# Kernel optimization log

Hardware: AMD Instinct MI355X
Metric: run time of the kernel (lower is better)

## Reference

```python
import jax, jax.numpy as jnp
import numpy as np

N = 100000      # total nodes across batched graphs
E = 1600000     # total edges (avg degree 16)
B = 4096        # number of graphs in the batch
DIM_IN = 74
D2 = 200
D3 = 12
H1 = 100        # gc1 output
DG = 20         # gc2 output (d_g)
M1 = 128
M2 = 32
FD = (DG + 1) * (D2 + 1)  # 4221 fusion features
EPS = 1e-5


def _glorot(k, shape):
    lim = float(np.sqrt(6.0 / (shape[0] + shape[1])))
    return jax.random.uniform(k, shape, jnp.float32, -lim, lim)


def setup_inputs() -> dict:
    key = jax.random.key(0)
    ks = jax.random.split(key, 18)
    inp = {
        'feat': jax.random.normal(ks[0], (N, DIM_IN), jnp.float32),
        'desc_2d': jax.random.normal(ks[1], (B, D2), jnp.float32),
        'desc_3d': jax.random.normal(ks[2], (B, D3), jnp.float32),
        'edge_src': jax.random.randint(ks[3], (E,), 0, N, jnp.int32),
        'edge_dst': jax.random.randint(ks[4], (E,), 0, N, jnp.int32),
        'graph_ids': jnp.sort(jax.random.randint(ks[5], (N,), 0, B, jnp.int32)),
        # GCN layer params (Linear inside NodeApplyModule)
        'W_gc1': _glorot(ks[6], (DIM_IN, H1)),
        'b_gc1': jnp.zeros((H1,), jnp.float32),
        'W_gc2': _glorot(ks[7], (H1, DG)),
        'b_gc2': jnp.zeros((DG,), jnp.float32),
        # attention weight W: (d_g, dim_2d_desc)
        'W_attn': _glorot(ks[8], (DG, D2)),
        # MLP
        'W_fc1': _glorot(ks[9], (FD, M1)),
        'b_fc1': jnp.zeros((M1,), jnp.float32),
        'W_fc2': _glorot(ks[10], (M1, M2)),
        'b_fc2': jnp.zeros((M2,), jnp.float32),
        'W_fc3': _glorot(ks[11], (M2, 1)),
        'b_fc3': jnp.zeros((1,), jnp.float32),
        # BatchNorm affine params
        'gamma1': jnp.ones((M1,), jnp.float32),
        'beta1': jnp.zeros((M1,), jnp.float32),
        'gamma2': jnp.ones((M2,), jnp.float32),
        'beta2': jnp.zeros((M2,), jnp.float32),
    }
    return inp


def _mean_agg(h, src, dst):
    # copy_u('h','m') then mean over mailbox; zero in-degree nodes keep h (DGL semantics)
    msg = h[src]                                                   # [E, d] gather
    s = jax.ops.segment_sum(msg, dst, num_segments=N)              # [N, d]
    deg = jax.ops.segment_sum(jnp.ones((src.shape[0],), h.dtype), dst, num_segments=N)
    mean = s / jnp.maximum(deg, 1.0)[:, None]
    return jnp.where((deg > 0)[:, None], mean, h)


def _batchnorm(x, gamma, beta):
    mu = jnp.mean(x, axis=0)
    var = jnp.mean(jnp.square(x - mu), axis=0)  # biased var (training mode)
    return (x - mu) * jax.lax.rsqrt(var + EPS) * gamma + beta


def reference(feat, desc_2d, desc_3d, edge_src, edge_dst, graph_ids,
              W_gc1, b_gc1, W_gc2, b_gc2, W_attn,
              W_fc1, b_fc1, W_fc2, b_fc2, W_fc3, b_fc3,
              gamma1, beta1, gamma2, beta2):
    # GCN layer 1: mean neighbor agg -> linear -> relu
    h = jax.nn.relu(_mean_agg(feat, edge_src, edge_dst) @ W_gc1 + b_gc1)   # [N, 100]
    # GCN layer 2
    h = jax.nn.relu(_mean_agg(h, edge_src, edge_dst) @ W_gc2 + b_gc2)      # [N, 20]
    # dgl.mean_nodes: per-graph mean readout
    sg = jax.ops.segment_sum(h, graph_ids, num_segments=B)                 # [B, 20]
    cnt = jax.ops.segment_sum(jnp.ones((N,), h.dtype), graph_ids, num_segments=B)
    hg = sg / jnp.maximum(cnt, 1.0)[:, None]                               # [B, 20]
    # attention over 2D descriptors
    attn = jax.nn.softmax(hg @ W_attn, axis=-1)                            # [B, 200]
    desc_att = attn * desc_2d
    # augment with ones and take outer product (bmm fusion)
    ones = jnp.ones((hg.shape[0], 1), hg.dtype)
    hg_a = jnp.concatenate([hg, ones], axis=1)                             # [B, 21]
    da_a = jnp.concatenate([desc_att, ones], axis=1)                       # [B, 201]
    fusion = jnp.einsum('bi,bj->bij', hg_a, da_a).reshape(hg.shape[0], -1) # [B, 4221]
    # MLP with BatchNorm (training-mode stats, dropout off)
    out = jax.nn.relu(_batchnorm(fusion @ W_fc1 + b_fc1, gamma1, beta1))
    out = jax.nn.relu(_batchnorm(out @ W_fc2 + b_fc2, gamma2, beta2))
    out = out @ W_fc3 + b_fc3                                              # [B, 1]
    return out
```

## Files before the change

### kernel.cpp

```cpp
#include <hip/hip_runtime.h>

#define NN 100000
#define NE 1600000
#define NB 4096
#define DIN 74
#define DPAD 80
#define DH1 100
#define DGD 20
#define DD2 200
#define DM1 128
#define DM2 32
#define NSEG 8
#define KPAD 4352
#define KSEG 544
#define NBUK 64
#define BNODES 1563
#define CAP 26500
#define EPB 3125
typedef unsigned int uint;
typedef unsigned short ushort;
typedef __attribute__((ext_vector_type(8))) short bf16x8;
typedef __attribute__((ext_vector_type(4))) float f32x4;

__device__ __forceinline__ float bf2f(ushort u){ return __uint_as_float(((uint)u)<<16); }
__device__ __forceinline__ ushort f2bf(float f){
  uint u = __float_as_uint(f);
  return (ushort)((u + 0x7fffu + ((u >> 16) & 1u)) >> 16);
}
__device__ __forceinline__ uint bucket_of(int d){
  return (uint)(((unsigned long long)(uint)d * 2747900ull) >> 32);
}
__device__ __forceinline__ void acc2u(float2& a, uint v){
  a.x += __uint_as_float(v << 16);
  a.y += __uint_as_float(v & 0xffff0000u);
}
__device__ __forceinline__ void acc8(float4& a, float4& b, uint4 v){
  a.x += __uint_as_float(v.x << 16);
  a.y += __uint_as_float(v.x & 0xffff0000u);
  a.z += __uint_as_float(v.y << 16);
  a.w += __uint_as_float(v.y & 0xffff0000u);
  b.x += __uint_as_float(v.z << 16);
  b.y += __uint_as_float(v.z & 0xffff0000u);
  b.z += __uint_as_float(v.w << 16);
  b.w += __uint_as_float(v.w & 0xffff0000u);
}

__global__ void k_cvt(const float* __restrict__ feat, const int* __restrict__ gid,
                      ushort* __restrict__ fb, int* __restrict__ cntg){
  int idx = blockIdx.x*256 + threadIdx.x;
  if(idx < NN*DPAD){
    int row = idx / DPAD, d = idx - row*DPAD;
    fb[idx] = (d < DIN) ? f2bf(feat[(size_t)row*DIN + d]) : (ushort)0;
  }
  if(idx < NN) atomicAdd(&cntg[gid[idx]], 1);
}

__global__ __launch_bounds__(256) void k_bucket2(const int* __restrict__ src,
      const int* __restrict__ dst, int* __restrict__ bukCur, uint2* __restrict__ pairs){
  __shared__ uint2 stage[EPB];
  __shared__ ushort bidx[EPB];
  __shared__ int cnt[NBUK], lofs[NBUK], gadj[NBUK], cur[NBUK];
  int tid = threadIdx.x;
  if(tid < NBUK) cnt[tid] = 0;
  __syncthreads();
  int e0 = blockIdx.x * EPB;
  for(int i = tid; i < EPB; i += 256)
    atomicAdd(&cnt[bucket_of(dst[e0 + i])], 1);
  __syncthreads();
  if(tid == 0){
    int acc = 0;
    #pragma unroll
    for(int b=0;b<NBUK;b++){ lofs[b] = acc; acc += cnt[b]; }
  }
  __syncthreads();
  if(tid < NBUK){
    int base = atomicAdd(&bukCur[tid], cnt[tid]);
    gadj[tid] = tid*CAP + base - lofs[tid];
    cur[tid]  = lofs[tid];
  }
  __syncthreads();
  for(int i = tid; i < EPB; i += 256){
    int d = dst[e0 + i];
    int s = src[e0 + i];
    uint b = bucket_of(d);
    int p = atomicAdd(&cur[b], 1);
    stage[p] = make_uint2((uint)s, (uint)d);
    bidx[p] = (ushort)b;
  }
  __syncthreads();
  for(int i = tid; i < EPB; i += 256)
    pairs[(size_t)gadj[bidx[i]] + i] = stage[i];
}

__global__ __launch_bounds__(512) void k_csr(const uint2* __restrict__ pairs,
      const int* __restrict__ bukTot, int* __restrict__ rowptr, int* __restrict__ adj){
  __shared__ int degL[BNODES];
  __shared__ int curL[BNODES];
  __shared__ int tsum[512];
  int b = blockIdx.x, tid = threadIdx.x;
  int d0 = b*BNODES;
  int nloc = min(BNODES, NN - d0);
  int gbase = 0;
  for(int i=0;i<b;i++) gbase += bukTot[i];
  int tot = bukTot[b];
  for(int i=tid;i<nloc;i+=512){ degL[i]=0; curL[i]=0; }
  __syncthreads();
  const uint2* pb = pairs + (size_t)b*CAP;
  for(int i=tid;i<tot;i+=512)
    atomicAdd(&degL[(int)pb[i].y - d0], 1);
  __syncthreads();
  int o0 = tid*4;
  int v0=0,v1=0,v2=0,v3=0,s=0;
  if(o0 < nloc){
    v0 = degL[o0];
    v1 = (o0+1<nloc)?degL[o0+1]:0;
    v2 = (o0+2<nloc)?degL[o0+2]:0;
    v3 = (o0+3<nloc)?degL[o0+3]:0;
    s = v0+v1+v2+v3;
  }
  tsum[tid]=s; __syncthreads();
  for(int off=1;off<512;off<<=1){
    int t2 = (tid>=off)?tsum[tid-off]:0;
    __syncthreads();
    tsum[tid]+=t2;
    __syncthreads();
  }
  int excl = tsum[tid]-s;
  if(o0 < nloc){
    int p0 = excl, p1 = p0+v0, p2 = p1+v1, p3 = p2+v2;
    degL[o0]=p0;
    rowptr[d0+o0]=gbase+p0;
    if(o0+1<nloc){ degL[o0+1]=p1; rowptr[d0+o0+1]=gbase+p1; }
    if(o0+2<nloc){ degL[o0+2]=p2; rowptr[d0+o0+2]=gbase+p2; }
    if(o0+3<nloc){ degL[o0+3]=p3; rowptr[d0+o0+3]=gbase+p3; }
  }
  if(b==NBUK-1 && tid==0) rowptr[NN]=gbase+tot;
  __syncthreads();
  for(int i=tid;i<tot;i+=512){
    uint2 pr = pb[i];
    int dl = (int)pr.y - d0;
    int pos = atomicAdd(&curL[dl],1);
    adj[gbase + degL[dl] + pos] = (int)pr.x;
  }
}

__global__ __launch_bounds__(512) void k_scan_g(const int* __restrict__ cntg,
                                                int* __restrict__ gofs){
  __shared__ int tsum[512];
  int tid = threadIdx.x;
  int o0 = tid*8;
  int v[8]; int s=0;
  #pragma unroll
  for(int j=0;j<8;j++){ v[j]=cntg[o0+j]; s+=v[j]; }
  tsum[tid]=s; __syncthreads();
  for(int off=1;off<512;off<<=1){
    int t=(tid>=off)?tsum[tid-off]:0;
    __syncthreads();
    tsum[tid]+=t;
    __syncthreads();
  }
  int acc = tsum[tid]-s;
  #pragma unroll
  for(int j=0;j<8;j++){ gofs[o0+j]=acc; acc+=v[j]; }
  if(tid==511) gofs[NB]=acc;
}

__global__ void k_agg1e(const ushort* __restrict__ fb, const float* __restrict__ feat,
                        const int* __restrict__ rowptr, const int* __restrict__ adj,
                        ushort* __restrict__ outb){
  int wid  = (blockIdx.x*blockDim.x + threadIdx.x) >> 6;
  int lane = threadIdx.x & 63;
  if(wid >= NN) return;
  int r0 = rowptr[wid], r1 = rowptr[wid+1];
  int eo = lane / 10;
  int part = lane - eo*10;
  bool act = lane < 60;
  if(!act){ eo = 0; part = 0; }
  float4 la0={0,0,0,0}, ha0={0,0,0,0}, la1={0,0,0,0}, ha1={0,0,0,0};
  float4 la2={0,0,0,0}, ha2={0,0,0,0}, la3={0,0,0,0}, ha3={0,0,0,0};
  for(int j = r0; j < r1; j += 24){
    int j0 = j + eo, j1 = j + 6 + eo, j2 = j + 12 + eo, j3 = j + 18 + eo;
    bool p0 = act && (j0 < r1), p1 = act && (j1 < r1);
    bool p2 = act && (j2 < r1), p3 = act && (j3 < r1);
    int s0 = adj[p0 ? j0 : r0];
    int s1 = adj[p1 ? j1 : r0];
    int s2 = adj[p2 ? j2 : r0];
    int s3 = adj[p3 ? j3 : r0];
    uint4 v0 = *(const uint4*)&fb[(size_t)s0*DPAD + part*8];
    uint4 v1 = *(const uint4*)&fb[(size_t)s1*DPAD + part*8];
    uint4 v2 = *(const uint4*)&fb[(size_t)s2*DPAD + part*8];
    uint4 v3 = *(const uint4*)&fb[(size_t)s3*DPAD + part*8];
    if(p0) acc8(la0, ha0, v0);
    if(p1) acc8(la1, ha1, v1);
    if(p2) acc8(la2, ha2, v2);
    if(p3) acc8(la3, ha3, v3);
  }
  float4 lo, hi;
  lo.x = (la0.x+la1.x)+(la2.x+la3.x); lo.y = (la0.y+la1.y)+(la2.y+la3.y);
  lo.z = (la0.z+la1.z)+(la2.z+la3.z); lo.w = (la0.w+la1.w)+(la2.w+la3.w);
  hi.x = (ha0.x+ha1.x)+(ha2.x+ha3.x); hi.y = (ha0.y+ha1.y)+(ha2.y+ha3.y);
  hi.z = (ha0.z+ha1.z)+(ha2.z+ha3.z); hi.w = (ha0.w+ha1.w)+(ha2.w+ha3.w);
  float4 L1,H1,L2,H2,L3,H3,L4,H4,L5,H5;
  #define SH4(dst,src,off) dst.x=__shfl(src.x,lane+off,64); dst.y=__shfl(src.y,lane+off,64); \
                           dst.z=__shfl(src.z,lane+off,64); dst.w=__shfl(src.w,lane+off,64);
  SH4(L1,lo,10) SH4(H1,hi,10)
  SH4(L2,lo,20) SH4(H2,hi,20)
  SH4(L3,lo,30) SH4(H3,hi,30)
  SH4(L4,lo,40) SH4(H4,hi,40)
  SH4(L5,lo,50) SH4(H5,hi,50)
  #undef SH4
  if(lane < 10){
    float4 tl, th;
    tl.x = ((lo.x+L1.x)+(L2.x+L3.x))+(L4.x+L5.x);
    tl.y = ((lo.y+L1.y)+(L2.y+L3.y))+(L4.y+L5.y);
    tl.z = ((lo.z+L1.z)+(L2.z+L3.z))+(L4.z+L5.z);
    tl.w = ((lo.w+L1.w)+(L2.w+L3.w))+(L4.w+L5.w);
    th.x = ((hi.x+H1.x)+(H2.x+H3.x))+(H4.x+H5.x);
    th.y = ((hi.y+H1.y)+(H2.y+H3.y))+(H4.y+H5.y);
    th.z = ((hi.z+H1.z)+(H2.z+H3.z))+(H4.z+H5.z);
    th.w = ((hi.w+H1.w)+(H2.w+H3.w))+(H4.w+H5.w);
    int d = r1 - r0;
    int dbase = part*8;
    if(d > 0){
      float inv = 1.f/(float)d;
      tl.x*=inv; tl.y*=inv; tl.z*=inv; tl.w*=inv;
      th.x*=inv; th.y*=inv; th.z*=inv; th.w*=inv;
    } else {
      const float* fr = feat + (size_t)wid*DIN;
      tl.x = (dbase+0 < DIN) ? fr[dbase+0] : 0.f;
      tl.y = (dbase+1 < DIN) ? fr[dbase+1] : 0.f;
      tl.z = (dbase+2 < DIN) ? fr[dbase+2] : 0.f;
      tl.w = (dbase+3 < DIN) ? fr[dbase+3] : 0.f;
      th.x = (dbase+4 < DIN) ? fr[dbase+4] : 0.f;
      th.y = (dbase+5 < DIN) ? fr[dbase+5] : 0.f;
      th.z = (dbase+6 < DIN) ? fr[dbase+6] : 0.f;
      th.w = (dbase+7 < DIN) ? fr[dbase+7] : 0.f;
    }
    uint4 o;
    o.x = (uint)f2bf(tl.x) | ((uint)f2bf(tl.y) << 16);
    o.y = (uint)f2bf(tl.z) | ((uint)f2bf(tl.w) << 16);
    o.z = (uint)f2bf(th.x) | ((uint)f2bf(th.y) << 16);
    o.w = (uint)f2bf(th.z) | ((uint)f2bf(th.w) << 16);
    *(uint4*)&outb[(size_t)wid*DPAD + dbase] = o;
  }
}

__global__ void k_prep_all(const float* __restrict__ Wf1, ushort* __restrict__ Bthi,
                           const float* __restrict__ W1g, ushort* __restrict__ W1tb,
                           const float* __restrict__ W2g, ushort* __restrict__ W2tb){
  int blk = blockIdx.x;
  int tid = threadIdx.x;
  if(blk < KPAD/32){
    __shared__ float Wl[32][128];
    int k0 = blk * 32;
    for(int idx=tid; idx<32*128; idx+=256){
      int kk = idx >> 7, n = idx & 127;
      int k = k0 + kk;
      Wl[kk][n] = (k < 4221) ? Wf1[(size_t)k*128 + n] : 0.f;
    }
    __syncthreads();
    int n = tid >> 1, kh = (tid & 1) * 16;
    uint ph[8];
    #pragma unroll
    for(int e=0;e<8;e++){
      ushort h0 = f2bf(Wl[kh+2*e][n]);
      ushort h1 = f2bf(Wl[kh+2*e+1][n]);
      ph[e] = (uint)h0 | ((uint)h1 << 16);
    }
    uint4* dh = (uint4*)(Bthi + (size_t)n*KPAD + k0 + kh);
    dh[0] = make_uint4(ph[0],ph[1],ph[2],ph[3]);
    dh[1] = make_uint4(ph[4],ph[5],ph[6],ph[7]);
  } else if(blk == KPAD/32){
    for(int idx = tid; idx < 112*96; idx += 256){
      int n = idx / 96, k = idx - n*96;
      float v = (n < DH1 && k < DIN) ? W1g[(size_t)k*DH1 + n] : 0.f;
      W1tb[idx] = f2bf(v);
    }
  } else {
    for(int idx = tid; idx < 32*128; idx += 256){
      int n = idx >> 7, k = idx & 127;
      float v = (n < DGD && k < DH1) ? W2g[(size_t)k*DGD + n] : 0.f;
      W2tb[idx] = f2bf(v);
    }
  }
}

__global__ __launch_bounds__(256) void k_gcn12(const ushort* __restrict__ Ab80,
      const ushort* __restrict__ W1tb, const ushort* __restrict__ W2tb,
      const float* __restrict__ b1, ushort* __restrict__ y2b){
  __shared__ ushort L[24960];
  ushort* As  = L;
  ushort* Ws  = L + 128*104;
  ushort* Hs  = L;
  ushort* W2s = L + 128*136;
  int tid = threadIdx.x;
  int n0 = blockIdx.x*128;
  #pragma unroll
  for(int p=0;p<5;p++){
    int idx = tid + p*256;
    int row = idx/10, c = (idx - row*10)*8;
    uint4 v = {0,0,0,0};
    if(n0+row < NN) v = *(const uint4*)&Ab80[(size_t)(n0+row)*DPAD + c];
    *(uint4*)&As[row*104 + c] = v;
  }
  { int row = tid>>1, c = 80 + (tid&1)*8;
    *(uint4*)&As[row*104 + c] = (uint4){0,0,0,0}; }
  #pragma unroll
  for(int p=0;p<6;p++){
    int idx = tid + p*256;
    if(idx < 1344){
      int row = idx/12, c = (idx - row*12)*8;
      *(uint4*)&Ws[row*104 + c] = *(const uint4*)&W1tb[row*96 + c];
    }
  }
  __syncthreads();
  int lane = tid & 63, w = tid >> 6;
  int wm = w*32;
  int frow = lane & 15, fk = (lane>>4)*8;
  f32x4 acc[2][7];
  #pragma unroll
  for(int a=0;a<2;a++)
    #pragma unroll
    for(int b=0;b<7;b++) acc[a][b] = (f32x4){0.f,0.f,0.f,0.f};
  #pragma unroll
  for(int ks=0; ks<3; ks++){
    bf16x8 af[2], bfr[7];
    #pragma unroll
    for(int mt=0;mt<2;mt++) af[mt] = *(const bf16x8*)&As[(wm+mt*16+frow)*104 + ks*32 + fk];
    #pragma unroll
    for(int nt=0;nt<7;nt++) bfr[nt] = *(const bf16x8*)&Ws[(nt*16+frow)*104 + ks*32 + fk];
    #pragma unroll
    for(int mt=0;mt<2;mt++)
      #pragma unroll
      for(int nt=0;nt<7;nt++)
        acc[mt][nt] = __builtin_amdgcn_mfma_f32_16x16x32_bf16(af[mt], bfr[nt], acc[mt][nt], 0, 0, 0);
  }
  int crow = (lane>>4)*4, ccol = lane & 15;
  float bv[7];
  #pragma unroll
  for(int nt=0;nt<7;nt++){
    int c = nt*16 + ccol;
    bv[nt] = (c < DH1) ? b1[c] : 0.f;
  }
  __syncthreads();
  #pragma unroll
  for(int mt=0;mt<2;mt++)
    #pragma unroll
    for(int nt=0;nt<7;nt++)
      #pragma unroll
      for(int rr=0;rr<4;rr++)
        Hs[(wm + mt*16 + crow + rr)*136 + nt*16 + ccol] =
            f2bf(fmaxf(acc[mt][nt][rr] + bv[nt], 0.f));
  { int row = tid>>1, c = 112 + (tid&1)*8;
    *(uint4*)&Hs[row*136 + c] = (uint4){0,0,0,0}; }
  #pragma unroll
  for(int p=0;p<2;p++){
    int idx = tid + p*256;
    int row = idx >> 4, c = (idx & 15)*8;
    *(uint4*)&W2s[row*136 + c] = *(const uint4*)&W2tb[row*128 + c];
  }
  __syncthreads();
  f32x4 acc2[2][2];
  #pragma unroll
  for(int a=0;a<2;a++){ acc2[a][0]=(f32x4){0,0,0,0}; acc2[a][1]=(f32x4){0,0,0,0}; }
  #pragma unroll
  for(int ks=0; ks<4; ks++){
    bf16x8 af2[2], bf2r[2];
    #pragma unroll
    for(int mt=0;mt<2;mt++) af2[mt] = *(const bf16x8*)&Hs[(wm+mt*16+frow)*136 + ks*32 + fk];
    #pragma unroll
    for(int nt=0;nt<2;nt++) bf2r[nt] = *(const bf16x8*)&W2s[(nt*16+frow)*136 + ks*32 + fk];
    #pragma unroll
    for(int mt=0;mt<2;mt++)
      #pragma unroll
      for(int nt=0;nt<2;nt++)
        acc2[mt][nt] = __builtin_amdgcn_mfma_f32_16x16x32_bf16(af2[mt], bf2r[nt], acc2[mt][nt], 0, 0, 0);
  }
  #pragma unroll
  for(int mt=0;mt<2;mt++)
    #pragma unroll
    for(int nt=0;nt<2;nt++)
      #pragma unroll
      for(int rr=0;rr<4;rr++){
        int col = nt*16 + ccol;
        int r = n0 + wm + mt*16 + crow + rr;
        if(col < DGD && r < NN)
          y2b[(size_t)r*DGD + col] = f2bf(acc2[mt][nt][rr]);
      }
}

__global__ void k_agg2d(const ushort* __restrict__ y2b, const int* __restrict__ rowptr,
                        const int* __restrict__ adj, const float* __restrict__ b2,
                        float* __restrict__ y3){
  int wid  = (blockIdx.x*blockDim.x + threadIdx.x) >> 6;
  int lane = threadIdx.x & 63;
  if(wid >= NN) return;
  int r0 = rowptr[wid], r1 = rowptr[wid+1];
  int eo = lane / 5;
  int part = lane - eo*5;
  bool act = lane < 60;
  if(!act){ eo = 0; part = 0; }
  float4 a0={0,0,0,0}, a1={0,0,0,0}, a2={0,0,0,0}, a3={0,0,0,0};
  for(int j = r0; j < r1; j += 48){
    int j0 = j + eo, j1 = j + 12 + eo, j2 = j + 24 + eo, j3 = j + 36 + eo;
    bool p0 = act && (j0 < r1), p1 = act && (j1 < r1);
    bool p2 = act && (j2 < r1), p3 = act && (j3 < r1);
    int s0 = adj[p0 ? j0 : r0];
    int s1 = adj[p1 ? j1 : r0];
    int s2 = adj[p2 ? j2 : r0];
    int s3 = adj[p3 ? j3 : r0];
    uint2 v0 = *(const uint2*)&y2b[(size_t)s0*DGD + part*4];
    uint2 v1 = *(const uint2*)&y2b[(size_t)s1*DGD + part*4];
    uint2 v2 = *(const uint2*)&y2b[(size_t)s2*DGD + part*4];
    uint2 v3 = *(const uint2*)&y2b[(size_t)s3*DGD + part*4];
    if(p0){ acc2u(*(float2*)&a0.x, v0.x); acc2u(*(float2*)&a0.z, v0.y); }
    if(p1){ acc2u(*(float2*)&a1.x, v1.x); acc2u(*(float2*)&a1.z, v1.y); }
    if(p2){ acc2u(*(float2*)&a2.x, v2.x); acc2u(*(float2*)&a2.z, v2.y); }
    if(p3){ acc2u(*(float2*)&a3.x, v3.x); acc2u(*(float2*)&a3.z, v3.y); }
  }
  float4 t;
  t.x = (a0.x+a1.x)+(a2.x+a3.x);
  t.y = (a0.y+a1.y)+(a2.y+a3.y);
  t.z = (a0.z+a1.z)+(a2.z+a3.z);
  t.w = (a0.w+a1.w)+(a2.w+a3.w);
  t.x += __shfl(t.x, lane+30, 64); t.y += __shfl(t.y, lane+30, 64);
  t.z += __shfl(t.z, lane+30, 64); t.w += __shfl(t.w, lane+30, 64);
  t.x += __shfl(t.x, lane+15, 64); t.y += __shfl(t.y, lane+15, 64);
  t.z += __shfl(t.z, lane+15, 64); t.w += __shfl(t.w, lane+15, 64);
  float ux = __shfl(t.x, lane+5, 64),  uy = __shfl(t.y, lane+5, 64);
  float uz = __shfl(t.z, lane+5, 64),  uw = __shfl(t.w, lane+5, 64);
  float wx = __shfl(t.x, lane+10, 64), wy = __shfl(t.y, lane+10, 64);
  float wz = __shfl(t.z, lane+10, 64), ww = __shfl(t.w, lane+10, 64);
  if(lane < 5){
    float tx = t.x + ux + wx, ty = t.y + uy + wy;
    float tz = t.z + uz + wz, tw = t.w + uw + ww;
    int d = r1 - r0;
    float bx, by, bz, bw;
    if(d > 0){
      float inv = 1.f/(float)d;
      bx = tx*inv; by = ty*inv; bz = tz*inv; bw = tw*inv;
    } else {
      uint2 v = *(const uint2*)&y2b[(size_t)wid*DGD + lane*4];
      bx = __uint_as_float(v.x << 16);
      by = __uint_as_float(v.x & 0xffff0000u);
      bz = __uint_as_float(v.y << 16);
      bw = __uint_as_float(v.y & 0xffff0000u);
    }
    float4 o;
    o.x = fmaxf(bx + b2[lane*4+0], 0.f);
    o.y = fmaxf(by + b2[lane*4+1], 0.f);
    o.z = fmaxf(bz + b2[lane*4+2], 0.f);
    o.w = fmaxf(bw + b2[lane*4+3], 0.f);
    *(float4*)&y3[(size_t)wid*DGD + lane*4] = o;
  }
}

__global__ __launch_bounds__(256) void k_head3(const float* __restrict__ y3,
      const int* __restrict__ gofs, const float* __restrict__ Wat,
      const float* __restrict__ desc2d, ushort* __restrict__ Ab){
  int g = blockIdx.x, t = threadIdx.x;
  int n0 = gofs[g], n1 = gofs[g+1];
  int cnt = n1 - n0;
  __shared__ float part[240];
  __shared__ float hgaL[21];
  __shared__ float daaL[201];
  __shared__ float red[256];
  if(t < 240){
    int grp = t/20, dim = t - grp*20;
    float a = 0.f;
    for(int n = n0 + grp; n < n1; n += 12) a += y3[(size_t)n*DGD + dim];
    part[t] = a;
  }
  __syncthreads();
  if(t < DGD){
    float s = 0.f;
    #pragma unroll
    for(int k=0;k<12;k++) s += part[k*20 + t];
    hgaL[t] = s / (float)max(cnt, 1);
  }
  if(t == DGD) hgaL[20] = 1.f;
  __syncthreads();
  float logit = 0.f;
  if(t < DD2){
    #pragma unroll
    for(int k=0;k<DGD;k++) logit += hgaL[k]*Wat[k*DD2 + t];
  }
  float v = (t < DD2) ? logit : -1e30f;
  red[t] = v; __syncthreads();
  for(int off=128; off>=1; off>>=1){ if(t<off) red[t]=fmaxf(red[t],red[t+off]); __syncthreads(); }
  float mx = red[0]; __syncthreads();
  float e = (t < DD2) ? expf(logit - mx) : 0.f;
  red[t] = e; __syncthreads();
  for(int off=128; off>=1; off>>=1){ if(t<off) red[t]+=red[t+off]; __syncthreads(); }
  float s = red[0];
  if(t < DD2) daaL[t] = (e/s)*desc2d[(size_t)g*DD2 + t];
  if(t == DD2) daaL[200] = 1.f;
  __syncthreads();
  ushort* arow = Ab + (size_t)g*KPAD;
  #pragma unroll
  for(int p=0;p<17;p++){
    int k = t + 256*p;
    ushort o = 0;
    if(k < 4221){
      int i = (int)(((uint)k * 83470u) >> 24);
      int j = k - i*201;
      o = f2bf(hgaL[i]*daaL[j]);
    }
    arow[k] = o;
  }
}

__global__ __launch_bounds__(256) void k_fuse6(const ushort* __restrict__ Ab,
                                               const ushort* __restrict__ Bthi,
                                               float* __restrict__ zp){
  __shared__ ushort Al[64][40];
  __shared__ ushort Bl[128][40];
  int tid = threadIdx.x;
  int m0 = blockIdx.x * 64;
  int seg = blockIdx.y;
  int lane = tid & 63;
  int w = tid >> 6;
  int wm = (w >> 1) * 32;
  int wn = (w & 1) * 64;
  f32x4 acc[2][4];
  #pragma unroll
  for(int a=0;a<2;a++)
    #pragma unroll
    for(int b=0;b<4;b++) acc[a][b] = (f32x4){0.f,0.f,0.f,0.f};

  int ar = tid >> 2;
  int as = (tid & 3) * 8;
  int br = tid >> 1;
  int bs = (tid & 1) * 16;
  const uint4* gA = (const uint4*)(Ab   + (size_t)(m0 + ar)*KPAD + seg*KSEG + as);
  const uint4* gB = (const uint4*)(Bthi + (size_t)br*KPAD + seg*KSEG + bs);

  int frow = lane & 15;
  int fk   = (lane >> 4) * 8;

  for(int ks=0; ks<17; ks++){
    uint4 va = gA[0];
    uint4 vb0 = gB[0], vb1 = gB[1];
    gA += 4; gB += 4;
    __syncthreads();
    *(uint4*)&Al[ar][as]   = va;
    *(uint4*)&Bl[br][bs]   = vb0;
    *(uint4*)&Bl[br][bs+8] = vb1;
    __syncthreads();
    bf16x8 af[2], bh[4];
    #pragma unroll
    for(int mt=0;mt<2;mt++) af[mt] = *(const bf16x8*)&Al[wm + mt*16 + frow][fk];
    #pragma unroll
    for(int nt=0;nt<4;nt++) bh[nt] = *(const bf16x8*)&Bl[wn + nt*16 + frow][fk];
    #pragma unroll
    for(int mt=0;mt<2;mt++)
      #pragma unroll
      for(int nt=0;nt<4;nt++)
        acc[mt][nt] = __builtin_amdgcn_mfma_f32_16x16x32_bf16(af[mt], bh[nt], acc[mt][nt], 0, 0, 0);
  }
  float* zb = zp + ((size_t)seg*NB + m0)*128;
  int drow = (lane >> 4) * 4;
  int dcol = lane & 15;
  #pragma unroll
  for(int mt=0;mt<2;mt++)
    #pragma unroll
    for(int nt=0;nt<4;nt++)
      #pragma unroll
      for(int rr=0;rr<4;rr++)
        zb[(size_t)(wm + mt*16 + drow + rr)*128 + wn + nt*16 + dcol] = acc[mt][nt][rr];
}

__global__ void k_reduce(const float* __restrict__ zp, const float* __restrict__ b1,
                         float* __restrict__ z1){
  int idx = blockIdx.x*256 + threadIdx.x;
  if(idx >= NB*32) return;
  const float4* z = (const float4*)zp;
  float4 o = ((const float4*)b1)[idx & 31];
  #pragma unroll
  for(int s=0;s<NSEG;s++){
    float4 a = z[idx + (size_t)s*NB*32];
    o.x += a.x; o.y += a.y; o.z += a.z; o.w += a.w;
  }
  ((float4*)z1)[idx] = o;
}

__global__ void k_bnstats(const float* __restrict__ X, int C,
                          const float* __restrict__ gamma, const float* __restrict__ beta,
                          float* __restrict__ scale, float* __restrict__ shift){
  int c = blockIdx.x;
  float s=0.f, s2=0.f;
  for(int r=threadIdx.x; r<NB; r+=256){
    float v = X[(size_t)r*C + c];
    s += v; s2 += v*v;
  }
  __shared__ float sh[256], sh2[256];
  sh[threadIdx.x]=s; sh2[threadIdx.x]=s2;
  __syncthreads();
  for(int off=128; off>=1; off>>=1){
    if(threadIdx.x<off){ sh[threadIdx.x]+=sh[threadIdx.x+off]; sh2[threadIdx.x]+=sh2[threadIdx.x+off]; }
    __syncthreads();
  }
  if(threadIdx.x==0){
    float mu  = sh[0]*(1.0f/NB);
    float var = sh2[0]*(1.0f/NB) - mu*mu;
    float a = gamma[c]*rsqrtf(var + 1e-5f);
    scale[c] = a;
    shift[c] = beta[c] - mu*a;
  }
}

__global__ void k_mlp2(const float* __restrict__ z1, const float* __restrict__ sc,
                       const float* __restrict__ sf, const float* __restrict__ W,
                       const float* __restrict__ bias, float* __restrict__ out){
  __shared__ float Wl[DM1*DM2];
  __shared__ float scl[DM1], sfl[DM1];
  for(int idx=threadIdx.x; idx<DM1*DM2; idx+=256) Wl[idx] = W[idx];
  if(threadIdx.x < DM1){ scl[threadIdx.x]=sc[threadIdx.x]; sfl[threadIdx.x]=sf[threadIdx.x]; }
  __syncthreads();
  int idx = blockIdx.x*256 + threadIdx.x;
  int r = idx >> 5, o = idx & 31;
  if(r >= NB) return;
  float acc = bias[o];
  const float* xr = z1 + (size_t)r*DM1;
  for(int k=0;k<DM1;k++){
    float xn = fmaxf(xr[k]*scl[k] + sfl[k], 0.f);
    acc += xn * Wl[k*DM2 + o];
  }
  out[(size_t)r*DM2 + o] = acc;
}

__global__ void k_final(const float* __restrict__ z2, const float* __restrict__ sc2,
                        const float* __restrict__ sf2, const float* __restrict__ W3,
                        const float* __restrict__ b3, float* __restrict__ out){
  int r = blockIdx.x*256 + threadIdx.x;
  if(r >= NB) return;
  float acc = b3[0];
  const float* xr = z2 + (size_t)r*DM2;
  #pragma unroll
  for(int o=0;o<DM2;o++){
    float xn = fmaxf(xr[o]*sc2[o] + sf2[o], 0.f);
    acc += xn * W3[o];
  }
  out[r] = acc;
}

extern "C" void kernel_launch(void* const* d_in, const int* in_sizes, int n_in,
                              void* d_out, int out_size, void* d_ws, size_t ws_size,
                              hipStream_t stream){
  (void)in_sizes; (void)n_in; (void)out_size; (void)ws_size;
  const float* feat   = (const float*)d_in[0];
  const float* desc2d = (const float*)d_in[1];
  const int*   esrc   = (const int*)d_in[3];
  const int*   edst   = (const int*)d_in[4];
  const int*   gid    = (const int*)d_in[5];
  const float* Wg1    = (const float*)d_in[6];
  const float* bg1    = (const float*)d_in[7];
  const float* Wg2    = (const float*)d_in[8];
  const float* bg2    = (const float*)d_in[9];
  const float* Wat    = (const float*)d_in[10];
  const float* Wf1    = (const float*)d_in[11];
  const float* bf1    = (const float*)d_in[12];
  const float* Wf2    = (const float*)d_in[13];
  const float* bf2    = (const float*)d_in[14];
  const float* Wf3    = (const float*)d_in[15];
  const float* bf3    = (const float*)d_in[16];
  const float* gamma1 = (const float*)d_in[17];
  const float* beta1  = (const float*)d_in[18];
  const float* gamma2 = (const float*)d_in[19];
  const float* beta2  = (const float*)d_in[20];
  float* out = (float*)d_out;

  char* base = (char*)d_ws;
  size_t off = 0;
  auto alloc = [&](size_t bytes)->void*{
    void* r = base + off;
    off = (off + bytes + 255) & ~(size_t)255;
    return r;
  };
  int*    rowptr = (int*)   alloc((size_t)(NN+1)*4);
  int*    cntg   = (int*)   alloc((size_t)NB*4);
  int*    gofs   = (int*)   alloc((size_t)(NB+1)*4);
  int*    adj    = (int*)   alloc((size_t)NE*4);
  int*    bukCur = (int*)   alloc((size_t)NBUK*4);
  float*  sc1    = (float*) alloc((size_t)DM1*4);
  float*  sf1    = (float*) alloc((size_t)DM1*4);
  float*  sc2    = (float*) alloc((size_t)DM2*4);
  float*  sf2    = (float*) alloc((size_t)DM2*4);
  ushort* W1thi  = (ushort*)alloc((size_t)128*KPAD*2);
  ushort* W1tb   = (ushort*)alloc((size_t)112*96*2);
  ushort* W2tb   = (ushort*)alloc((size_t)32*128*2);
  float*  z1     = (float*) alloc((size_t)NB*DM1*4);
  float*  z2     = (float*) alloc((size_t)NB*DM2*4);
  char*   R1     = (char*)  alloc((size_t)NN*DPAD*4);
  char*   R2     = (char*)  alloc((size_t)NB*KPAD*2);
  uint2*  pairs  = (uint2*) R1;
  ushort* agg80b = (ushort*)R1;
  float*  zp     = (float*) R1;
  float*  y3     = (float*) (R1 + (size_t)17*1024*1024);
  ushort* featb  = (ushort*)R2;
  ushort* y2b    = (ushort*)(R2 + (size_t)NN*DPAD*2);
  ushort* Ab     = (ushort*)R2;

  hipMemsetAsync(cntg,   0, (size_t)NB*4, stream);
  hipMemsetAsync(bukCur, 0, (size_t)NBUK*4, stream);

  k_cvt    <<<(NN*DPAD+255)/256, 256, 0, stream>>>(feat, gid, featb, cntg);
  k_bucket2<<<512, 256, 0, stream>>>(esrc, edst, bukCur, pairs);
  k_csr    <<<NBUK, 512, 0, stream>>>(pairs, bukCur, rowptr, adj);
  k_scan_g <<<1, 512, 0, stream>>>(cntg, gofs);

  k_prep_all<<<KPAD/32 + 2, 256, 0, stream>>>(Wf1, W1thi, Wg1, W1tb, Wg2, W2tb);
  k_agg1e <<<(NN+3)/4, 256, 0, stream>>>(featb, feat, rowptr, adj, agg80b);
  k_gcn12 <<<(NN+127)/128, 256, 0, stream>>>(agg80b, W1tb, W2tb, bg1, y2b);
  k_agg2d <<<(NN+3)/4, 256, 0, stream>>>(y2b, rowptr, adj, bg2, y3);

  k_head3<<<NB, 256, 0, stream>>>(y3, gofs, Wat, desc2d, Ab);
  k_fuse6<<<dim3(64, NSEG), 256, 0, stream>>>(Ab, W1thi, zp);
  k_reduce<<<(NB*32+255)/256, 256, 0, stream>>>(zp, bf1, z1);

  k_bnstats<<<DM1, 256, 0, stream>>>(z1, DM1, gamma1, beta1, sc1, sf1);
  k_mlp2   <<<(NB*DM2)/256, 256, 0, stream>>>(z1, sc1, sf1, Wf2, bf2, z2);
  k_bnstats<<<DM2, 256, 0, stream>>>(z2, DM2, gamma2, beta2, sc2, sf2);
  k_final  <<<(NB+255)/256, 256, 0, stream>>>(z2, sc2, sf2, Wf3, bf3, out);
}
```

Measured before the change: 260.6 us.

## Merge preprocessing kernels into one launch and compute graph offsets by binary search

```diff
diff --git a/kernel.cpp b/kernel.cpp
--- a/kernel.cpp
+++ b/kernel.cpp
@@ -17,6 +17,9 @@
 #define BNODES 1563
 #define CAP 26500
 #define EPB 3125
+#define PRE_BUK 512
+#define PRE_PREP (KPAD/32 + 2)
+#define PRE_CVT ((NN*DPAD+255)/256)
 typedef unsigned int uint;
 typedef unsigned short ushort;
 typedef __attribute__((ext_vector_type(8))) short bf16x8;
@@ -45,55 +48,107 @@
   b.w += __uint_as_float(v.w & 0xffff0000u);
 }
 
-__global__ void k_cvt(const float* __restrict__ feat, const int* __restrict__ gid,
-                      ushort* __restrict__ fb, int* __restrict__ cntg){
-  int idx = blockIdx.x*256 + threadIdx.x;
-  if(idx < NN*DPAD){
-    int row = idx / DPAD, d = idx - row*DPAD;
-    fb[idx] = (d < DIN) ? f2bf(feat[(size_t)row*DIN + d]) : (ushort)0;
-  }
-  if(idx < NN) atomicAdd(&cntg[gid[idx]], 1);
-}
-
-__global__ __launch_bounds__(256) void k_bucket2(const int* __restrict__ src,
-      const int* __restrict__ dst, int* __restrict__ bukCur, uint2* __restrict__ pairs){
-  __shared__ uint2 stage[EPB];
-  __shared__ ushort bidx[EPB];
-  __shared__ int cnt[NBUK], lofs[NBUK], gadj[NBUK], cur[NBUK];
-  int tid = threadIdx.x;
-  if(tid < NBUK) cnt[tid] = 0;
-  __syncthreads();
-  int e0 = blockIdx.x * EPB;
-  for(int i = tid; i < EPB; i += 256)
-    atomicAdd(&cnt[bucket_of(dst[e0 + i])], 1);
-  __syncthreads();
-  if(tid == 0){
-    int acc = 0;
-    #pragma unroll
-    for(int b=0;b<NBUK;b++){ lofs[b] = acc; acc += cnt[b]; }
-  }
-  __syncthreads();
-  if(tid < NBUK){
-    int base = atomicAdd(&bukCur[tid], cnt[tid]);
-    gadj[tid] = tid*CAP + base - lofs[tid];
-    cur[tid]  = lofs[tid];
-  }
-  __syncthreads();
-  for(int i = tid; i < EPB; i += 256){
-    int d = dst[e0 + i];
-    int s = src[e0 + i];
-    uint b = bucket_of(d);
-    int p = atomicAdd(&cur[b], 1);
-    stage[p] = make_uint2((uint)s, (uint)d);
-    bidx[p] = (ushort)b;
-  }
-  __syncthreads();
-  for(int i = tid; i < EPB; i += 256)
-    pairs[(size_t)gadj[bidx[i]] + i] = stage[i];
-}
-
-__global__ __launch_bounds__(512) void k_csr(const uint2* __restrict__ pairs,
-      const int* __restrict__ bukTot, int* __restrict__ rowptr, int* __restrict__ adj){
+__global__ __launch_bounds__(256) void k_pre(
+      const int* __restrict__ src, const int* __restrict__ dst,
+      int* __restrict__ bukCur, uint2* __restrict__ pairs,
+      const float* __restrict__ Wf1, ushort* __restrict__ Bthi,
+      const float* __restrict__ W1g, ushort* __restrict__ W1tb,
+      const float* __restrict__ W2g, ushort* __restrict__ W2tb,
+      const float* __restrict__ feat, ushort* __restrict__ fb){
+  __shared__ __align__(16) char SM[32384];
+  int blk = blockIdx.x, tid = threadIdx.x;
+  if(blk < PRE_BUK){
+    uint2* stage = (uint2*)SM;
+    ushort* bidx = (ushort*)(SM + 25000);
+    int* cnt  = (int*)(SM + 31252);
+    int* lofs = cnt + NBUK;
+    int* gadj = lofs + NBUK;
+    int* cur  = gadj + NBUK;
+    if(tid < NBUK) cnt[tid] = 0;
+    __syncthreads();
+    int e0 = blk * EPB;
+    for(int i = tid; i < EPB; i += 256)
+      atomicAdd(&cnt[bucket_of(dst[e0 + i])], 1);
+    __syncthreads();
+    if(tid == 0){
+      int acc = 0;
+      #pragma unroll
+      for(int b=0;b<NBUK;b++){ lofs[b] = acc; acc += cnt[b]; }
+    }
+    __syncthreads();
+    if(tid < NBUK){
+      int base = atomicAdd(&bukCur[tid], cnt[tid]);
+      gadj[tid] = tid*CAP + base - lofs[tid];
+      cur[tid]  = lofs[tid];
+    }
+    __syncthreads();
+    for(int i = tid; i < EPB; i += 256){
+      int d = dst[e0 + i];
+      int s = src[e0 + i];
+      uint b = bucket_of(d);
+      int p = atomicAdd(&cur[b], 1);
+      stage[p] = make_uint2((uint)s, (uint)d);
+      bidx[p] = (ushort)b;
+    }
+    __syncthreads();
+    for(int i = tid; i < EPB; i += 256)
+      pairs[(size_t)gadj[bidx[i]] + i] = stage[i];
+  } else if(blk < PRE_BUK + KPAD/32){
+    float (*Wl)[128] = (float(*)[128])SM;
+    int k0 = (blk - PRE_BUK) * 32;
+    for(int idx=tid; idx<32*128; idx+=256){
+      int kk = idx >> 7, n = idx & 127;
+      int k = k0 + kk;
+      Wl[kk][n] = (k < 4221) ? Wf1[(size_t)k*128 + n] : 0.f;
+    }
+    __syncthreads();
+    int n = tid >> 1, kh = (tid & 1) * 16;
+    uint ph[8];
+    #pragma unroll
+    for(int e=0;e<8;e++){
+      ushort h0 = f2bf(Wl[kh+2*e][n]);
+      ushort h1 = f2bf(Wl[kh+2*e+1][n]);
+      ph[e] = (uint)h0 | ((uint)h1 << 16);
+    }
+    uint4* dh = (uint4*)(Bthi + (size_t)n*KPAD + k0 + kh);
+    dh[0] = make_uint4(ph[0],ph[1],ph[2],ph[3]);
+    dh[1] = make_uint4(ph[4],ph[5],ph[6],ph[7]);
+  } else if(blk == PRE_BUK + KPAD/32){
+    for(int idx = tid; idx < 112*96; idx += 256){
+      int n = idx / 96, k = idx - n*96;
+      float v = (n < DH1 && k < DIN) ? W1g[(size_t)k*DH1 + n] : 0.f;
+      W1tb[idx] = f2bf(v);
+    }
+  } else if(blk == PRE_BUK + KPAD/32 + 1){
+    for(int idx = tid; idx < 32*128; idx += 256){
+      int n = idx >> 7, k = idx & 127;
+      float v = (n < DGD && k < DH1) ? W2g[(size_t)k*DGD + n] : 0.f;
+      W2tb[idx] = f2bf(v);
+    }
+  } else {
+    int idx = (blk - (PRE_BUK + PRE_PREP))*256 + tid;
+    if(idx < NN*DPAD){
+      int row = idx / DPAD, d = idx - row*DPAD;
+      fb[idx] = (d < DIN) ? f2bf(feat[(size_t)row*DIN + d]) : (ushort)0;
+    }
+  }
+}
+
+__global__ __launch_bounds__(512) void k_csr2(const uint2* __restrict__ pairs,
+      const int* __restrict__ bukTot, int* __restrict__ rowptr, int* __restrict__ adj,
+      const int* __restrict__ gid, int* __restrict__ gofs){
+  if(blockIdx.x == NBUK){
+    int tid = threadIdx.x;
+    for(int g = tid; g <= NB; g += 512){
+      int lo = 0, hi = NN;
+      while(lo < hi){
+        int mid = (lo + hi) >> 1;
+        if(gid[mid] < g) lo = mid + 1; else hi = mid;
+      }
+      gofs[g] = lo;
+    }
+    return;
+  }
   __shared__ int degL[BNODES];
   __shared__ int curL[BNODES];
   __shared__ int tsum[512];
@@ -142,27 +197,6 @@
     int pos = atomicAdd(&curL[dl],1);
     adj[gbase + degL[dl] + pos] = (int)pr.x;
   }
-}
-
-__global__ __launch_bounds__(512) void k_scan_g(const int* __restrict__ cntg,
-                                                int* __restrict__ gofs){
-  __shared__ int tsum[512];
-  int tid = threadIdx.x;
-  int o0 = tid*8;
-  int v[8]; int s=0;
-  #pragma unroll
-  for(int j=0;j<8;j++){ v[j]=cntg[o0+j]; s+=v[j]; }
-  tsum[tid]=s; __syncthreads();
-  for(int off=1;off<512;off<<=1){
-    int t=(tid>=off)?tsum[tid-off]:0;
-    __syncthreads();
-    tsum[tid]+=t;
-    __syncthreads();
-  }
-  int acc = tsum[tid]-s;
-  #pragma unroll
-  for(int j=0;j<8;j++){ gofs[o0+j]=acc; acc+=v[j]; }
-  if(tid==511) gofs[NB]=acc;
 }
 
 __global__ void k_agg1e(const ushort* __restrict__ fb, const float* __restrict__ feat,
@@ -245,46 +279,6 @@
   }
 }
 
-__global__ void k_prep_all(const float* __restrict__ Wf1, ushort* __restrict__ Bthi,
-                           const float* __restrict__ W1g, ushort* __restrict__ W1tb,
-                           const float* __restrict__ W2g, ushort* __restrict__ W2tb){
-  int blk = blockIdx.x;
-  int tid = threadIdx.x;
-  if(blk < KPAD/32){
-    __shared__ float Wl[32][128];
-    int k0 = blk * 32;
-    for(int idx=tid; idx<32*128; idx+=256){
-      int kk = idx >> 7, n = idx & 127;
-      int k = k0 + kk;
-      Wl[kk][n] = (k < 4221) ? Wf1[(size_t)k*128 + n] : 0.f;
-    }
-    __syncthreads();
-    int n = tid >> 1, kh = (tid & 1) * 16;
-    uint ph[8];
-    #pragma unroll
-    for(int e=0;e<8;e++){
-      ushort h0 = f2bf(Wl[kh+2*e][n]);
-      ushort h1 = f2bf(Wl[kh+2*e+1][n]);
-      ph[e] = (uint)h0 | ((uint)h1 << 16);
-    }
-    uint4* dh = (uint4*)(Bthi + (size_t)n*KPAD + k0 + kh);
-    dh[0] = make_uint4(ph[0],ph[1],ph[2],ph[3]);
-    dh[1] = make_uint4(ph[4],ph[5],ph[6],ph[7]);
-  } else if(blk == KPAD/32){
-    for(int idx = tid; idx < 112*96; idx += 256){
-      int n = idx / 96, k = idx - n*96;
-      float v = (n < DH1 && k < DIN) ? W1g[(size_t)k*DH1 + n] : 0.f;
-      W1tb[idx] = f2bf(v);
-    }
-  } else {
-    for(int idx = tid; idx < 32*128; idx += 256){
-      int n = idx >> 7, k = idx & 127;
-      float v = (n < DGD && k < DH1) ? W2g[(size_t)k*DGD + n] : 0.f;
-      W2tb[idx] = f2bf(v);
-    }
-  }
-}
-
 __global__ __launch_bounds__(256) void k_gcn12(const ushort* __restrict__ Ab80,
       const ushort* __restrict__ W1tb, const ushort* __restrict__ W2tb,
       const float* __restrict__ b1, ushort* __restrict__ y2b){
@@ -678,7 +672,6 @@
     return r;
   };
   int*    rowptr = (int*)   alloc((size_t)(NN+1)*4);
-  int*    cntg   = (int*)   alloc((size_t)NB*4);
   int*    gofs   = (int*)   alloc((size_t)(NB+1)*4);
   int*    adj    = (int*)   alloc((size_t)NE*4);
   int*    bukCur = (int*)   alloc((size_t)NBUK*4);
@@ -701,15 +694,12 @@
   ushort* y2b    = (ushort*)(R2 + (size_t)NN*DPAD*2);
   ushort* Ab     = (ushort*)R2;
 
-  hipMemsetAsync(cntg,   0, (size_t)NB*4, stream);
   hipMemsetAsync(bukCur, 0, (size_t)NBUK*4, stream);
 
-  k_cvt    <<<(NN*DPAD+255)/256, 256, 0, stream>>>(feat, gid, featb, cntg);
-  k_bucket2<<<512, 256, 0, stream>>>(esrc, edst, bukCur, pairs);
-  k_csr    <<<NBUK, 512, 0, stream>>>(pairs, bukCur, rowptr, adj);
-  k_scan_g <<<1, 512, 0, stream>>>(cntg, gofs);
-
-  k_prep_all<<<KPAD/32 + 2, 256, 0, stream>>>(Wf1, W1thi, Wg1, W1tb, Wg2, W2tb);
+  k_pre <<<PRE_BUK + PRE_PREP + PRE_CVT, 256, 0, stream>>>(
+      esrc, edst, bukCur, pairs, Wf1, W1thi, Wg1, W1tb, Wg2, W2tb, feat, featb);
+  k_csr2<<<NBUK + 1, 512, 0, stream>>>(pairs, bukCur, rowptr, adj, gid, gofs);
+
   k_agg1e <<<(NN+3)/4, 256, 0, stream>>>(featb, feat, rowptr, adj, agg80b);
   k_gcn12 <<<(NN+127)/128, 256, 0, stream>>>(agg80b, W1tb, W2tb, bg1, y2b);
   k_agg2d <<<(NN+3)/4, 256, 0, stream>>>(y2b, rowptr, adj, bg2, y3);
```

Measured after the change: 242.8 us. -6.9%, faster.
